# Kernel optimization log

Measured on AMD Instinct MI355X. Metric: run time of the kernel, lower is better.

## Reference

```python
import jax, jax.numpy as jnp
import numpy as np

NUM_HEADS = 16
D_MODEL = 1024
SEQ = 4096
HEAD_DIM = D_MODEL // NUM_HEADS
ROPE_BASE = 10000.0


def _rope(x):
    # x: [h, s, d]  (rotate-half RoPE per head)
    s, d = x.shape[-2], x.shape[-1]
    inv_freq = 1.0 / (ROPE_BASE ** (jnp.arange(0, d, 2, dtype=jnp.float32) / d))  # [d/2]
    ang = jnp.arange(s, dtype=jnp.float32)[:, None] * inv_freq[None, :]           # [s, d/2]
    cos, sin = jnp.cos(ang), jnp.sin(ang)
    x1, x2 = x[..., : d // 2], x[..., d // 2 :]
    return jnp.concatenate([x1 * cos - x2 * sin, x1 * sin + x2 * cos], axis=-1)


def setup_inputs() -> dict:
    key = jax.random.key(0)
    kq, kk, kv, kwq, kwk, kwv = jax.random.split(key, 6)
    scale = 1.0 / np.sqrt(D_MODEL)
    return {
        "q": jax.random.normal(kq, (SEQ, D_MODEL), dtype=jnp.float32),
        "k": jax.random.normal(kk, (SEQ, D_MODEL), dtype=jnp.float32),
        "v": jax.random.normal(kv, (SEQ, D_MODEL), dtype=jnp.float32),
        "mask": jnp.tril(jnp.ones((SEQ, SEQ), dtype=bool)),  # causal
        "Wq": jax.random.normal(kwq, (D_MODEL, D_MODEL), dtype=jnp.float32) * scale,
        "Wk": jax.random.normal(kwk, (D_MODEL, D_MODEL), dtype=jnp.float32) * scale,
        "Wv": jax.random.normal(kwv, (D_MODEL, D_MODEL), dtype=jnp.float32) * scale,
    }


def reference(q, k, v, mask, Wq, Wk, Wv):
    # Projections (eqx Linear: x @ W.T, no bias)
    qp = q @ Wq.T  # [s, d_model]
    kp = k @ Wk.T
    vp = v @ Wv.T
    # split heads: [s, (h d)] -> [h, s, d]
    def split(x):
        return x.reshape(SEQ, NUM_HEADS, HEAD_DIM).transpose(1, 0, 2)
    qh, kh, vh = split(qp), split(kp), split(vp)
    qh = _rope(qh)
    kh = _rope(kh)
    # explicit full logits, masked softmax (matches original, no SDPA)
    logits = jnp.einsum("hqd,hkd->hqk", qh, kh) / jnp.sqrt(jnp.float32(HEAD_DIM))
    logits = jnp.where(mask[None, :, :], logits, -jnp.inf)
    attn = jax.nn.softmax(logits, axis=-1)  # [h, q, k]
    out = jnp.einsum("hqk,hkd->hqd", attn, vh)
    return out.transpose(1, 0, 2).reshape(SEQ, D_MODEL)
```

## Files before the change

kernel.cpp:

```cpp
#include <hip/hip_runtime.h>
#include <math.h>

#define SEQ 4096
#define DMODEL 1024
#define NHEADS 16
#define HDIM 64

typedef __bf16 v8bf __attribute__((ext_vector_type(8)));
typedef float f32x4 __attribute__((ext_vector_type(4)));
typedef float f32x16 __attribute__((ext_vector_type(16)));
typedef int i32x2 __attribute__((ext_vector_type(2)));
typedef int i32x4 __attribute__((ext_vector_type(4)));

#define NPART 4608
#define SCALE_Q 0.18033688011112042f

__device__ __forceinline__ unsigned short f2bf(float f) {
    union { float f; unsigned int u; } v; v.f = f;
    unsigned int u = v.u;
    return (unsigned short)((u + 0x7fffu + ((u >> 16) & 1u)) >> 16);
}

__device__ __forceinline__ int cvtpk(float lo, float hi) {
    int r;
    asm("v_cvt_pk_bf16_f32 %0, %1, %2" : "=v"(r) : "v"(lo), "v"(hi));
    return r;
}

__device__ __forceinline__ void gload16(const unsigned short* g, unsigned short* l) {
    __builtin_amdgcn_global_load_lds(
        (const __attribute__((address_space(1))) unsigned int*)g,
        (__attribute__((address_space(3))) unsigned int*)l, 16, 0, 0);
}

__global__ __launch_bounds__(256) void cast_kernel(
    const float* __restrict__ q, const float* __restrict__ k, const float* __restrict__ v,
    const float* __restrict__ wq, const float* __restrict__ wk, const float* __restrict__ wv,
    unsigned short* __restrict__ xq, unsigned short* __restrict__ xk,
    unsigned short* __restrict__ xv, unsigned short* __restrict__ wb)
{
    const size_t M4 = (size_t)4 << 20, M1 = (size_t)1 << 20;
    size_t i = ((size_t)blockIdx.x * 256 + threadIdx.x) * 8;
    const float* s; unsigned short* d; size_t off;
    if (i < M4)                 { s = q;  d = xq;          off = i; }
    else if (i < 2 * M4)        { s = k;  d = xk;          off = i - M4; }
    else if (i < 3 * M4)        { s = v;  d = xv;          off = i - 2 * M4; }
    else if (i < 3 * M4 + M1)   { s = wq; d = wb;          off = i - 3 * M4; }
    else if (i < 3 * M4 + 2*M1) { s = wk; d = wb + M1;     off = i - 3 * M4 - M1; }
    else                        { s = wv; d = wb + 2 * M1; off = i - 3 * M4 - 2 * M1; }
    float4 a = *reinterpret_cast<const float4*>(s + off);
    float4 b = *reinterpret_cast<const float4*>(s + off + 4);
    uint4 u;
    u.x = (unsigned)cvtpk(a.x, a.y); u.y = (unsigned)cvtpk(a.z, a.w);
    u.z = (unsigned)cvtpk(b.x, b.y); u.w = (unsigned)cvtpk(b.z, b.w);
    *reinterpret_cast<uint4*>(d + off) = u;
}

__global__ __launch_bounds__(256) void proj_rope_kernel(
    const unsigned short* __restrict__ Xq, const unsigned short* __restrict__ Xk,
    const unsigned short* __restrict__ Xv, const unsigned short* __restrict__ Wb,
    unsigned short* __restrict__ qh, unsigned short* __restrict__ kfr,
    unsigned short* __restrict__ vfr)
{
    const int tz = blockIdx.z;
    const unsigned short* __restrict__ X = (tz == 0) ? Xq : (tz == 1) ? Xk : Xv;
    const unsigned short* __restrict__ W = Wb + (size_t)tz * ((size_t)1 << 20);

    const int tid = threadIdx.x;
    const int lane = tid & 63;
    const int wid = tid >> 6;
    const int l15 = lane & 15;
    const int l4 = lane >> 4;
    const int wr = wid >> 1, wc = wid & 1;

    const int m0 = blockIdx.x * 128;
    const int n0 = blockIdx.y * 128;

    __shared__ __align__(16) unsigned short Ab[2][4096];
    __shared__ __align__(16) unsigned short Bb[2][4096];

    int grow[2], gcol[2];
    #pragma unroll
    for (int g = 0; g < 2; ++g) {
        int row = wid * 32 + g * 16 + (lane >> 2);
        grow[g] = row;
        gcol[g] = 8 * ((lane & 3) ^ ((row >> 1) & 3));
    }

    auto STAGE = [&](int b, int kt) {
        const int k0 = kt << 5;
        #pragma unroll
        for (int g = 0; g < 2; ++g) {
            gload16(X + (size_t)(m0 + grow[g]) * DMODEL + k0 + gcol[g],
                    &Ab[b][(wid * 2 + g) * 512]);
            gload16(W + (size_t)(n0 + grow[g]) * DMODEL + k0 + gcol[g],
                    &Bb[b][(wid * 2 + g) * 512]);
        }
    };

    f32x4 acc[4][4] = {};

    STAGE(0, 0);
    for (int kt = 0; kt < 32; ++kt) {
        __syncthreads();
        if (kt < 31) STAGE((kt + 1) & 1, kt + 1);

        const unsigned short* A = Ab[kt & 1];
        const unsigned short* B = Bb[kt & 1];

        v8bf af[4], bfr[4];
        #pragma unroll
        for (int mi = 0; mi < 4; ++mi) {
            int row = wr * 64 + mi * 16 + l15;
            int byte = row * 64 + ((l4 ^ ((row >> 1) & 3)) << 4);
            af[mi] = *reinterpret_cast<const v8bf*>(reinterpret_cast<const char*>(A) + byte);
        }
        #pragma unroll
        for (int ni = 0; ni < 4; ++ni) {
            int row = wc * 64 + ni * 16 + l15;
            int byte = row * 64 + ((l4 ^ ((row >> 1) & 3)) << 4);
            bfr[ni] = *reinterpret_cast<const v8bf*>(reinterpret_cast<const char*>(B) + byte);
        }
        #pragma unroll
        for (int mi = 0; mi < 4; ++mi)
            #pragma unroll
            for (int ni = 0; ni < 4; ++ni)
                acc[mi][ni] = __builtin_amdgcn_mfma_f32_16x16x32_bf16(af[mi], bfr[ni], acc[mi][ni], 0, 0, 0);
    }

    const int h = (n0 >> 6) + wc;
    const int mbase = m0 + wr * 64;
    const int T = blockIdx.x * 2 + wr;

    if (tz == 2) {
        unsigned short* vb = vfr + (size_t)h * 262144 + (size_t)T * 4096;
        #pragma unroll
        for (int mi = 0; mi < 4; ++mi) {
            #pragma unroll
            for (int ni = 0; ni < 4; ++ni) {
                int f = (ni >> 1) * 4 + mi;
                int off = f * 512 + ((l4 >> 1) * 32 + (ni & 1) * 16 + l15) * 8 + (l4 & 1) * 4;
                uint2 pk;
                pk.x = (unsigned)cvtpk(acc[mi][ni][0], acc[mi][ni][1]);
                pk.y = (unsigned)cvtpk(acc[mi][ni][2], acc[mi][ni][3]);
                *reinterpret_cast<uint2*>(vb + off) = pk;
            }
        }
    } else if (tz == 1) {
        unsigned short* kb = kfr + (size_t)h * 262144 + (size_t)T * 4096;
        #pragma unroll
        for (int ni = 0; ni < 2; ++ni) {
            int j = ni * 16 + l15;
            float invf = expf(-(float)j * 0.28782313662425574f);
            #pragma unroll
            for (int mi = 0; mi < 4; ++mi) {
                #pragma unroll
                for (int r = 0; r < 4; ++r) {
                    int m = mbase + mi * 16 + l4 * 4 + r;
                    float ang = (float)m * invf;
                    float sn, cs;
                    sincosf(ang, &sn, &cs);
                    float x1 = acc[mi][ni][r];
                    float x2 = acc[mi][ni + 2][r];
                    int rowoff = ((l15 >> 3) * 32 + (mi & 1) * 16 + l4 * 4 + r) * 8 + (l15 & 7);
                    int fb = (mi >> 1) * 4;
                    kb[(fb + ni) * 512 + rowoff]     = f2bf(x1 * cs - x2 * sn);
                    kb[(fb + ni + 2) * 512 + rowoff] = f2bf(x1 * sn + x2 * cs);
                }
            }
        }
    } else {
        unsigned short* base = qh + (size_t)h * SEQ * HDIM;
        #pragma unroll
        for (int ni = 0; ni < 2; ++ni) {
            int j = ni * 16 + l15;
            float invf = expf(-(float)j * 0.28782313662425574f);
            #pragma unroll
            for (int mi = 0; mi < 4; ++mi) {
                #pragma unroll
                for (int r = 0; r < 4; ++r) {
                    int m = mbase + mi * 16 + l4 * 4 + r;
                    float ang = (float)m * invf;
                    float sn, cs;
                    sincosf(ang, &sn, &cs);
                    sn *= SCALE_Q; cs *= SCALE_Q;
                    float x1 = acc[mi][ni][r];
                    float x2 = acc[mi][ni + 2][r];
                    base[(size_t)m * HDIM + j]      = f2bf(x1 * cs - x2 * sn);
                    base[(size_t)m * HDIM + j + 32] = f2bf(x1 * sn + x2 * cs);
                }
            }
        }
    }
}

__global__ __launch_bounds__(256, 2) void attn_kernel(
    const unsigned short* __restrict__ qh, const unsigned short* __restrict__ kfr,
    const unsigned short* __restrict__ vfr, float* __restrict__ out,
    unsigned short* __restrict__ po, float* __restrict__ ml)
{
    const int tid = threadIdx.x;
    const int lane = tid & 63;
    const int wid = tid >> 6;
    const int l31 = lane & 31;
    const int l5 = lane >> 5;

    const int bid = blockIdx.x;
    const int xcd = bid & 7;
    const int idx = bid >> 3;
    const int c4 = idx * 4 + wid;
    const int hsel = (c4 >= 320) ? 1 : 0;
    const int h = (xcd << 1) | hsel;
    const int r = 319 - (c4 - hsel * 320);

    int qb, c, nc;
    if (r < 32)       { qb = r;                     c = 0;            nc = 1; }
    else if (r < 96)  { qb = 32 + ((r - 32) >> 1);  c = (r - 32) & 1; nc = 2; }
    else if (r < 192) { int rr = r - 96; qb = 64 + rr / 3; c = rr - (qb - 64) * 3; nc = 3; }
    else              { int rr = r - 192; qb = 96 + (rr >> 2); c = rr & 3; nc = 4; }

    const int q0 = qb * 32;
    const int q = q0 + l31;
    const int nt = (q0 + 32 + 63) >> 6;
    const int t0 = c * 16;
    const int t1 = min(t0 + 16, nt);

    const unsigned short* __restrict__ qbase = qh + ((size_t)h * SEQ + q) * HDIM + l5 * 8;
    const unsigned short* __restrict__ kfh = kfr + (size_t)h * 262144 + lane * 8;
    const unsigned short* __restrict__ vfh = vfr + (size_t)h * 262144 + lane * 8;

    v8bf qf[4];
    #pragma unroll
    for (int dk = 0; dk < 4; ++dk)
        qf[dk] = *reinterpret_cast<const v8bf*>(qbase + dk * 16);

    f32x16 of[2] = {};
    float lreg = 0.0f;

    auto LOADK = [&](v8bf (&KB)[8], int T) {
        const unsigned short* kp = kfh + (size_t)T * 4096;
        #pragma unroll
        for (int f = 0; f < 8; ++f)
            KB[f] = *reinterpret_cast<const v8bf*>(kp + f * 512);
    };

    auto ROUND = [&](int T, v8bf (&KC)[8], v8bf (&KN)[8]) {
        v8bf vf[8];
        {
            const unsigned short* vp = vfh + (size_t)T * 4096;
            #pragma unroll
            for (int f = 0; f < 8; ++f)
                vf[f] = *reinterpret_cast<const v8bf*>(vp + f * 512);
        }
        if (T + 1 < t1) LOADK(KN, T + 1);

        f32x16 st[2];
        __builtin_amdgcn_s_setprio(1);
        #pragma unroll
        for (int ns = 0; ns < 2; ++ns) {
            f32x16 acc = {};
            #pragma unroll
            for (int dk = 0; dk < 4; ++dk)
                acc = __builtin_amdgcn_mfma_f32_32x32x16_bf16(KC[ns * 4 + dk], qf[dk], acc, 0, 0, 0);
            st[ns] = acc;
        }
        __builtin_amdgcn_s_setprio(0);

        if (T == nt - 1) {
            const int kvb = T * 64 + 4 * l5;
            #pragma unroll
            for (int ns = 0; ns < 2; ++ns)
                #pragma unroll
                for (int i = 0; i < 16; ++i) {
                    int kv = kvb + ns * 32 + (i & 3) + 8 * (i >> 2);
                    if (kv > q) st[ns][i] = -INFINITY;
                }
        }

        float ps0 = 0.f, ps1 = 0.f, ps2 = 0.f, ps3 = 0.f;
        #pragma unroll
        for (int ns = 0; ns < 2; ++ns)
            #pragma unroll
            for (int i = 0; i < 16; ++i) {
                float p = exp2f(st[ns][i]);
                st[ns][i] = p;
                if ((i & 3) == 0) ps0 += p; else if ((i & 3) == 1) ps1 += p;
                else if ((i & 3) == 2) ps2 += p; else ps3 += p;
            }
        lreg += (ps0 + ps1) + (ps2 + ps3);

        v8bf pt[4];
        #pragma unroll
        for (int kb = 0; kb < 4; ++kb) {
            int ns = kb >> 1, kp = (kb & 1) * 8;
            int A0 = cvtpk(st[ns][kp + 0], st[ns][kp + 1]);
            int A1 = cvtpk(st[ns][kp + 2], st[ns][kp + 3]);
            int B0 = cvtpk(st[ns][kp + 4], st[ns][kp + 5]);
            int B1 = cvtpk(st[ns][kp + 6], st[ns][kp + 7]);
            i32x2 s0 = __builtin_amdgcn_permlane32_swap(A0, B0, false, false);
            i32x2 s1 = __builtin_amdgcn_permlane32_swap(A1, B1, false, false);
            i32x4 u; u.x = s0.x; u.y = s1.x; u.z = s0.y; u.w = s1.y;
            v8bf p; __builtin_memcpy(&p, &u, 16);
            pt[kb] = p;
        }

        __builtin_amdgcn_s_setprio(1);
        #pragma unroll
        for (int dt = 0; dt < 2; ++dt)
            #pragma unroll
            for (int kb = 0; kb < 4; ++kb)
                of[dt] = __builtin_amdgcn_mfma_f32_32x32x16_bf16(vf[dt * 4 + kb], pt[kb], of[dt], 0, 0, 0);
        __builtin_amdgcn_s_setprio(0);
    };

    v8bf kA[8], kB[8];
    LOADK(kA, t0);
    int t = t0;
    while (true) {
        ROUND(t, kA, kB);
        if (++t == t1) break;
        ROUND(t, kB, kA);
        if (++t == t1) break;
    }

    {
        i32x2 sw = __builtin_amdgcn_permlane32_swap(__float_as_int(lreg), __float_as_int(lreg), false, false);
        lreg = __int_as_float(sw.x) + __int_as_float(sw.y);
    }

    if (nc == 1) {
        float inv = 1.0f / lreg;
        float* obase = out + (size_t)q * DMODEL + h * HDIM + l5 * 4;
        #pragma unroll
        for (int dt = 0; dt < 2; ++dt)
            #pragma unroll
            for (int g = 0; g < 4; ++g) {
                f32x4 o4;
                o4[0] = of[dt][g * 4 + 0] * inv;
                o4[1] = of[dt][g * 4 + 1] * inv;
                o4[2] = of[dt][g * 4 + 2] * inv;
                o4[3] = of[dt][g * 4 + 3] * inv;
                *reinterpret_cast<f32x4*>(obase + dt * 32 + g * 8) = o4;
            }
    } else {
        const int p = h * 288 + (r - 32);
        unsigned short* pb = po + ((size_t)p * 32 + l31) * 64 + l5 * 4;
        #pragma unroll
        for (int dt = 0; dt < 2; ++dt)
            #pragma unroll
            for (int g = 0; g < 4; ++g) {
                uint2 u;
                u.x = (unsigned)cvtpk(of[dt][g * 4 + 0], of[dt][g * 4 + 1]);
                u.y = (unsigned)cvtpk(of[dt][g * 4 + 2], of[dt][g * 4 + 3]);
                *reinterpret_cast<uint2*>(pb + dt * 32 + g * 8) = u;
            }
        if (l5 == 0) {
            float2 v; v.x = 0.0f; v.y = lreg;
            reinterpret_cast<float2*>(ml)[(size_t)p * 32 + l31] = v;
        }
    }
}

__global__ __launch_bounds__(256) void combine_kernel(
    const unsigned short* __restrict__ po, const float* __restrict__ ml,
    float* __restrict__ out)
{
    const int b = blockIdx.x;
    const int h = b / 96;
    const int j = b - h * 96;
    const int qb = 32 + j;
    int nc, r0;
    if (qb < 64)      { nc = 2; r0 = 32 + ((qb - 32) << 1); }
    else if (qb < 96) { nc = 3; r0 = 96 + (qb - 64) * 3; }
    else              { nc = 4; r0 = 192 + ((qb - 96) << 2); }
    const int p0 = h * 288 + (r0 - 32);
    const int d = threadIdx.x & 63;
    const int rg = threadIdx.x >> 6;
    const int q0 = qb * 32;

    for (int row = rg; row < 32; row += 4) {
        float L = 0.0f, O = 0.0f;
        #pragma unroll
        for (int ci = 0; ci < 4; ++ci)
            if (ci < nc) {
                float2 v = reinterpret_cast<const float2*>(ml)[(size_t)(p0 + ci) * 32 + row];
                L += v.y;
                unsigned int raw = po[((size_t)(p0 + ci) * 32 + row) * 64 + d];
                union { unsigned int u; float f; } cv; cv.u = raw << 16;
                O += cv.f;
            }
        out[(size_t)(q0 + row) * DMODEL + h * HDIM + d] = O / L;
    }
}

extern "C" void kernel_launch(void* const* d_in, const int* in_sizes, int n_in,
                              void* d_out, int out_size, void* d_ws, size_t ws_size,
                              hipStream_t stream) {
    (void)in_sizes; (void)n_in; (void)out_size; (void)ws_size;
    const float* q  = (const float*)d_in[0];
    const float* k  = (const float*)d_in[1];
    const float* v  = (const float*)d_in[2];
    const float* Wq = (const float*)d_in[4];
    const float* Wk = (const float*)d_in[5];
    const float* Wv = (const float*)d_in[6];

    const size_t M4 = (size_t)4 << 20;
    unsigned short* qh  = (unsigned short*)d_ws;
    unsigned short* kfr = qh  + M4;
    unsigned short* vfr = kfr + M4;
    unsigned short* scratch = vfr + M4;
    unsigned short* Xbv = scratch;
    unsigned short* Wb  = scratch + M4;
    unsigned short* po  = scratch;
    float* ml = (float*)(po + (size_t)NPART * 32 * 64);
    unsigned short* Xbq = (unsigned short*)d_out;
    unsigned short* Xbk = Xbq + M4;
    float* out = (float*)d_out;

    cast_kernel<<<dim3(7680), 256, 0, stream>>>(q, k, v, Wq, Wk, Wv, Xbq, Xbk, Xbv, Wb);

    dim3 g1(SEQ / 128, DMODEL / 128, 3);
    proj_rope_kernel<<<g1, 256, 0, stream>>>(Xbq, Xbk, Xbv, Wb, qh, kfr, vfr);

    attn_kernel<<<dim3(1280), 256, 0, stream>>>(qh, kfr, vfr, out, po, ml);

    combine_kernel<<<dim3(16 * 96), 256, 0, stream>>>(po, ml, out);
}
```

Measured before the change: 147.2 us.

## Precompute RoPE cos/sin table and compute softmax row sums via MFMA with ones

Adds a small kernel that precomputes a cos/sin table for all positions and frequencies, so the projection epilogue reads from the table instead of calling sincosf and expf per element. In the attention kernel, the per-row softmax denominator is now accumulated by an extra MFMA of a ones vector against the bf16 probability tiles. This replaces the scalar VALU adds and the cross-lane permlane reduction. The trade is an extra kernel launch plus global table reads, and four extra MFMAs per round. The row sum now comes from bf16-rounded probabilities, matching what is multiplied into V.

Measured after the change: 149.4 us. No clear change (+1.5%).

```diff
diff --git a/kernel.cpp b/kernel.cpp
--- a/kernel.cpp
+++ b/kernel.cpp
@@ -56,9 +56,22 @@
     *reinterpret_cast<uint4*>(d + off) = u;
 }
 
+__global__ __launch_bounds__(256) void rope_table_kernel(float2* __restrict__ tab)
+{
+    int idx = blockIdx.x * 256 + threadIdx.x;
+    int m = idx >> 5;
+    int j = idx & 31;
+    float invf = expf(-(float)j * 0.28782313662425574f);
+    float sn, cs;
+    sincosf((float)m * invf, &sn, &cs);
+    float2 t; t.x = cs; t.y = sn;
+    tab[idx] = t;
+}
+
 __global__ __launch_bounds__(256) void proj_rope_kernel(
     const unsigned short* __restrict__ Xq, const unsigned short* __restrict__ Xk,
     const unsigned short* __restrict__ Xv, const unsigned short* __restrict__ Wb,
+    const float2* __restrict__ rope_tab,
     unsigned short* __restrict__ qh, unsigned short* __restrict__ kfr,
     unsigned short* __restrict__ vfr)
 {
@@ -151,15 +164,13 @@
         #pragma unroll
         for (int ni = 0; ni < 2; ++ni) {
             int j = ni * 16 + l15;
-            float invf = expf(-(float)j * 0.28782313662425574f);
             #pragma unroll
             for (int mi = 0; mi < 4; ++mi) {
                 #pragma unroll
                 for (int r = 0; r < 4; ++r) {
                     int m = mbase + mi * 16 + l4 * 4 + r;
-                    float ang = (float)m * invf;
-                    float sn, cs;
-                    sincosf(ang, &sn, &cs);
+                    float2 t = rope_tab[m * 32 + j];
+                    float cs = t.x, sn = t.y;
                     float x1 = acc[mi][ni][r];
                     float x2 = acc[mi][ni + 2][r];
                     int rowoff = ((l15 >> 3) * 32 + (mi & 1) * 16 + l4 * 4 + r) * 8 + (l15 & 7);
@@ -174,16 +185,13 @@
         #pragma unroll
         for (int ni = 0; ni < 2; ++ni) {
             int j = ni * 16 + l15;
-            float invf = expf(-(float)j * 0.28782313662425574f);
             #pragma unroll
             for (int mi = 0; mi < 4; ++mi) {
                 #pragma unroll
                 for (int r = 0; r < 4; ++r) {
                     int m = mbase + mi * 16 + l4 * 4 + r;
-                    float ang = (float)m * invf;
-                    float sn, cs;
-                    sincosf(ang, &sn, &cs);
-                    sn *= SCALE_Q; cs *= SCALE_Q;
+                    float2 t = rope_tab[m * 32 + j];
+                    float cs = t.x * SCALE_Q, sn = t.y * SCALE_Q;
                     float x1 = acc[mi][ni][r];
                     float x2 = acc[mi][ni + 2][r];
                     base[(size_t)m * HDIM + j]      = f2bf(x1 * cs - x2 * sn);
@@ -234,8 +242,14 @@
     for (int dk = 0; dk < 4; ++dk)
         qf[dk] = *reinterpret_cast<const v8bf*>(qbase + dk * 16);
 
+    v8bf onesf;
+    {
+        i32x4 o; o.x = 0x3F803F80; o.y = 0x3F803F80; o.z = 0x3F803F80; o.w = 0x3F803F80;
+        __builtin_memcpy(&onesf, &o, 16);
+    }
+
     f32x16 of[2] = {};
-    float lreg = 0.0f;
+    f32x16 lacc = {};
 
     auto LOADK = [&](v8bf (&KB)[8], int T) {
         const unsigned short* kp = kfh + (size_t)T * 4096;
@@ -277,17 +291,11 @@
                 }
         }
 
-        float ps0 = 0.f, ps1 = 0.f, ps2 = 0.f, ps3 = 0.f;
         #pragma unroll
         for (int ns = 0; ns < 2; ++ns)
             #pragma unroll
-            for (int i = 0; i < 16; ++i) {
-                float p = exp2f(st[ns][i]);
-                st[ns][i] = p;
-                if ((i & 3) == 0) ps0 += p; else if ((i & 3) == 1) ps1 += p;
-                else if ((i & 3) == 2) ps2 += p; else ps3 += p;
-            }
-        lreg += (ps0 + ps1) + (ps2 + ps3);
+            for (int i = 0; i < 16; ++i)
+                st[ns][i] = exp2f(st[ns][i]);
 
         v8bf pt[4];
         #pragma unroll
@@ -310,6 +318,9 @@
             #pragma unroll
             for (int kb = 0; kb < 4; ++kb)
                 of[dt] = __builtin_amdgcn_mfma_f32_32x32x16_bf16(vf[dt * 4 + kb], pt[kb], of[dt], 0, 0, 0);
+        #pragma unroll
+        for (int kb = 0; kb < 4; ++kb)
+            lacc = __builtin_amdgcn_mfma_f32_32x32x16_bf16(onesf, pt[kb], lacc, 0, 0, 0);
         __builtin_amdgcn_s_setprio(0);
     };
 
@@ -323,13 +334,10 @@
         if (++t == t1) break;
     }
 
-    {
-        i32x2 sw = __builtin_amdgcn_permlane32_swap(__float_as_int(lreg), __float_as_int(lreg), false, false);
-        lreg = __int_as_float(sw.x) + __int_as_float(sw.y);
-    }
+    const float lsum = lacc[0];
 
     if (nc == 1) {
-        float inv = 1.0f / lreg;
+        float inv = 1.0f / lsum;
         float* obase = out + (size_t)q * DMODEL + h * HDIM + l5 * 4;
         #pragma unroll
         for (int dt = 0; dt < 2; ++dt)
@@ -355,7 +363,7 @@
                 *reinterpret_cast<uint2*>(pb + dt * 32 + g * 8) = u;
             }
         if (l5 == 0) {
-            float2 v; v.x = 0.0f; v.y = lreg;
+            float2 v; v.x = 0.0f; v.y = lsum;
             reinterpret_cast<float2*>(ml)[(size_t)p * 32 + l31] = v;
         }
     }
@@ -411,6 +419,7 @@
     unsigned short* scratch = vfr + M4;
     unsigned short* Xbv = scratch;
     unsigned short* Wb  = scratch + M4;
+    float2* rope_tab = (float2*)(Wb + 3 * ((size_t)1 << 20));
     unsigned short* po  = scratch;
     float* ml = (float*)(po + (size_t)NPART * 32 * 64);
     unsigned short* Xbq = (unsigned short*)d_out;
@@ -418,9 +427,10 @@
     float* out = (float*)d_out;
 
     cast_kernel<<<dim3(7680), 256, 0, stream>>>(q, k, v, Wq, Wk, Wv, Xbq, Xbk, Xbv, Wb);
+    rope_table_kernel<<<dim3(512), 256, 0, stream>>>(rope_tab);
 
     dim3 g1(SEQ / 128, DMODEL / 128, 3);
-    proj_rope_kernel<<<g1, 256, 0, stream>>>(Xbq, Xbk, Xbv, Wb, qh, kfr, vfr);
+    proj_rope_kernel<<<g1, 256, 0, stream>>>(Xbq, Xbk, Xbv, Wb, rope_tab, qh, kfr, vfr);
 
     attn_kernel<<<dim3(1280), 256, 0, stream>>>(qh, kfr, vfr, out, po, ml);
 
```
